# Kernel tuning notes

Hardware: AMD Instinct MI355X
Metric: run time of the kernel (lower is better)

The kernel has to match this reference:

```python
import jax, jax.numpy as jnp
import numpy as np

EMB = 512
QKV = 512
H = 8      # num_heads
PH = 8     # num_pheads
HD = QKV // H
PHD = QKV // PH


def _make_params(key):
    names = ['Wi', 'Wip', 'Wic', 'Wq', 'Wpq', 'Wk', 'Wpk', 'Wv', 'Wpv', 'Wo', 'Wop']
    ks = jax.random.split(key, len(names))
    p = {}
    for n, k in zip(names, ks):
        din = EMB if n in ('Wi', 'Wip', 'Wic') else QKV
        dout = EMB if n in ('Wo', 'Wop') else QKV
        p[n] = jax.random.normal(k, (din, dout), jnp.float32) * 0.02
        p['b' + n[1:]] = jnp.zeros((dout,), jnp.float32)
    return p


def setup_inputs() -> dict:
    key = jax.random.key(0)
    kq, kp, kc, kw = jax.random.split(key, 4)
    B, S, P = 16, 4096, 64
    inp = {
        'query': jax.random.normal(kq, (B, S, EMB), jnp.float32),
        'pquery': jax.random.normal(kp, (B, P, EMB), jnp.float32),
        'context': jax.random.normal(kc, (B, S, EMB), jnp.float32),
    }
    inp.update(_make_params(kw))
    return inp


def reference(query, pquery, context,
              Wi, bi, Wip, bip, Wic, bic,
              Wq, bq, Wpq, bpq, Wk, bk, Wpk, bpk,
              Wv, bv, Wpv, bpv, Wo, bo, Wop, bop):
    # Dropout layers act as identity (eval mode / deterministic reference).
    B, S, _ = query.shape
    P = pquery.shape[1]

    q_in = query @ Wi + bi        # (B,S,QKV)
    pq_in = pquery @ Wip + bip    # (B,P,QKV)
    c_in = context @ Wic + bic    # (B,S,QKV)

    # --- pack stage: pquery attends over context -> p_context ---
    pq = ((pq_in @ Wpq + bpq) * (PHD ** -0.5)).reshape(B, P, PH, PHD)
    pk = (c_in @ Wpk + bpk).reshape(B, S, PH, PHD)
    pv = (c_in @ Wpv + bpv).reshape(B, S, PH, PHD)
    # dropout before softmax in original; identity here
    pattn = jax.nn.softmax(jnp.einsum('bphd,bshd->bhps', pq, pk), axis=-1)
    pc = jnp.einsum('bhps,bshd->bphd', pattn, pv).reshape(B, P, QKV)

    # --- unpack stage: query attends over p_context ---
    q = ((q_in @ Wq + bq) * (HD ** -0.5)).reshape(B, S, H, HD)
    k = (pc @ Wk + bk).reshape(B, P, H, HD)
    v = (pc @ Wv + bv).reshape(B, P, H, HD)
    aw = jax.nn.softmax(jnp.einsum('bshd,bphd->bhsp', q, k), axis=-1)  # (B,H,S,P)
    attn = jnp.einsum('bhsp,bphd->bshd', aw, v).reshape(B, S, QKV)
    attn = attn @ Wo + bo           # (B,S,EMB)
    pc_out = pc @ Wop + bop         # (B,P,EMB)

    # torch returns attn_weights as (S, B*H, P) when batch_first
    aw_t = jnp.transpose(aw.reshape(B * H, S, P), (1, 0, 2))
    return attn, pc_out, aw_t
```

## Files before the change

kernel.cpp:

```cpp
#include <hip/hip_runtime.h>


typedef __bf16 bf16x8 __attribute__((ext_vector_type(8)));
typedef float f32x4 __attribute__((ext_vector_type(4)));
typedef unsigned short u16x8 __attribute__((ext_vector_type(8)));
typedef unsigned short u16x4 __attribute__((ext_vector_type(4)));

#define MFMA16(a, b, c) __builtin_amdgcn_mfma_f32_16x16x32_bf16((a), (b), (c), 0, 0, 0)

__device__ __forceinline__ unsigned short f2bf_bits(float f) {
  unsigned int u = __float_as_uint(f);
  u += 0x7fffu + ((u >> 16) & 1u);
  return (unsigned short)(u >> 16);
}

__device__ __forceinline__ void gload16(const unsigned short* g, unsigned short* l) {
  __builtin_amdgcn_global_load_lds(
      (const __attribute__((address_space(1))) void*)g,
      (__attribute__((address_space(3))) void*)l, 16, 0, 0);
}

struct Ptr8 { const float* p[8]; };

__global__ __launch_bounds__(256) void transpose_w8(Ptr8 srcs,
                                                    unsigned short* __restrict__ WT) {
  const float* __restrict__ W = srcs.p[blockIdx.z];
  unsigned short* __restrict__ O = WT + (size_t)blockIdx.z * 262144;
  __shared__ float tile[32][33];
  const int t = threadIdx.x;
  const int tr = blockIdx.x * 32, tc = blockIdx.y * 32;
  {
    const int r = t >> 3, c4 = (t & 7) * 4;
    const float4 v = *reinterpret_cast<const float4*>(&W[(size_t)(tr + r) * 512 + tc + c4]);
    tile[r][c4 + 0] = v.x; tile[r][c4 + 1] = v.y; tile[r][c4 + 2] = v.z; tile[r][c4 + 3] = v.w;
  }
  __syncthreads();
  {
    const int n = t >> 3, k4 = (t & 7) * 4;
    u16x4 o;
#pragma unroll
    for (int j = 0; j < 4; j++) o[j] = f2bf_bits(tile[k4 + j][n]);
    *reinterpret_cast<u16x4*>(&O[(size_t)(tc + n) * 512 + tr + k4]) = o;
  }
}

__global__ __launch_bounds__(256) void bias_all(
    const float* bi, const float* bip, const float* bic,
    const float* Wq, const float* Wpq, const float* Wpk, const float* Wpv,
    const float* bq, const float* bpq, const float* bpk, const float* bpv,
    float* __restrict__ out) {
  const int y = blockIdx.y;
  const float* bin  = (y == 0) ? bi : (y == 1) ? bip : bic;
  const float* W    = (y == 0) ? Wq : (y == 1) ? Wpq : (y == 2) ? Wpk : Wpv;
  const float* bout = (y == 0) ? bq : (y == 1) ? bpq : (y == 2) ? bpk : bpv;
  const float scale = (y < 2) ? 0.125f : 1.0f;
  const int n = blockIdx.x * 256 + threadIdx.x;
  float s = 0.f;
  for (int k = 0; k < 512; k++) s += bin[k] * W[(size_t)k * 512 + n];
  out[y * 512 + n] = (s + bout[n]) * scale;
}

__global__ __launch_bounds__(256) void gemm_wcomb(
    const float* __restrict__ Wi, const float* __restrict__ Wip,
    const float* __restrict__ Wic, const unsigned short* __restrict__ WTbase,
    unsigned short* __restrict__ outbase) {
  const int z = blockIdx.z;
  const float* __restrict__ A = (z == 0) ? Wi : (z == 1) ? Wip : Wic;
  const unsigned short* __restrict__ BT = WTbase + (size_t)z * 262144;
  unsigned short* __restrict__ out = outbase + (size_t)z * 262144;
  const float scale = (z < 2) ? 0.125f : 1.0f;

  __shared__ __align__(16) unsigned short As[128 * 72];
  __shared__ __align__(16) unsigned short Bs[128 * 72];
  const int t = threadIdx.x;
  const int w = t >> 6, l = t & 63, li = l & 15, lg = l >> 4;
  const int wm = w >> 1, wn = w & 1;
  const int m0 = blockIdx.x * 128, n0 = blockIdx.y * 128;

  f32x4 acc[4][4] = {};

  for (int kt = 0; kt < 512; kt += 64) {
#pragma unroll
    for (int i = 0; i < 8; i++) {
      const int row = i * 16 + (t >> 4), k = (t & 15) * 4;
      const float4 v = *reinterpret_cast<const float4*>(&A[(size_t)(m0 + row) * 512 + kt + k]);
      u16x4 o;
      o[0] = f2bf_bits(v.x); o[1] = f2bf_bits(v.y);
      o[2] = f2bf_bits(v.z); o[3] = f2bf_bits(v.w);
      *reinterpret_cast<u16x4*>(&As[row * 72 + k]) = o;
    }
#pragma unroll
    for (int i = 0; i < 4; i++) {
      const int row = i * 32 + (t >> 3), k = (t & 7) * 8;
      const u16x8 v = *reinterpret_cast<const u16x8*>(&BT[(size_t)(n0 + row) * 512 + kt + k]);
      *reinterpret_cast<u16x8*>(&Bs[row * 72 + k]) = v;
    }
    __syncthreads();
#pragma unroll
    for (int kk = 0; kk < 2; kk++) {
      bf16x8 a[4], b[4];
#pragma unroll
      for (int mf = 0; mf < 4; mf++)
        a[mf] = *reinterpret_cast<const bf16x8*>(&As[(wm * 64 + mf * 16 + li) * 72 + kk * 32 + lg * 8]);
#pragma unroll
      for (int nf = 0; nf < 4; nf++)
        b[nf] = *reinterpret_cast<const bf16x8*>(&Bs[(wn * 64 + nf * 16 + li) * 72 + kk * 32 + lg * 8]);
#pragma unroll
      for (int mf = 0; mf < 4; mf++)
#pragma unroll
        for (int nf = 0; nf < 4; nf++)
          acc[mf][nf] = MFMA16(a[mf], b[nf], acc[mf][nf]);
    }
    __syncthreads();
  }
  const int lg4 = lg * 4;
#pragma unroll
  for (int nf = 0; nf < 4; nf++) {
    const int col = n0 + wn * 64 + nf * 16 + li;
#pragma unroll
    for (int mf = 0; mf < 4; mf++) {
      const int row = m0 + wm * 64 + mf * 16 + lg4;
#pragma unroll
      for (int r = 0; r < 4; r++)
        out[(size_t)col * 512 + row + r] = f2bf_bits(acc[mf][nf][r] * scale);
    }
  }
}

__global__ __launch_bounds__(256) void conv_bf16(const float* __restrict__ q,
                                                 const float* __restrict__ c,
                                                 unsigned short* __restrict__ qo,
                                                 unsigned short* __restrict__ co) {
  const float* __restrict__ src = blockIdx.y ? c : q;
  unsigned short* __restrict__ dst = blockIdx.y ? co : qo;
#pragma unroll
  for (int i = 0; i < 8; i++) {
    const size_t idx = (((size_t)i * 2048 + blockIdx.x) * 256 + threadIdx.x) * 8;
    const float4 v0 = *reinterpret_cast<const float4*>(&src[idx]);
    const float4 v1 = *reinterpret_cast<const float4*>(&src[idx + 4]);
    u16x8 o;
    o[0] = f2bf_bits(v0.x); o[1] = f2bf_bits(v0.y); o[2] = f2bf_bits(v0.z); o[3] = f2bf_bits(v0.w);
    o[4] = f2bf_bits(v1.x); o[5] = f2bf_bits(v1.y); o[6] = f2bf_bits(v1.z); o[7] = f2bf_bits(v1.w);
    *reinterpret_cast<u16x8*>(&dst[idx]) = o;
  }
}

template <int MODE>
__global__ __launch_bounds__(256) void gemm_bf16(
    const unsigned short* __restrict__ A, const unsigned short* __restrict__ BT,
    const float* __restrict__ bias0, const float* __restrict__ bias1,
    const float* __restrict__ bias2, void* out0, void* out1, void* out2,
    int K, int Ntiles, int ldc) {
  __shared__ __align__(16) unsigned short As[128 * 64];
  __shared__ __align__(16) unsigned short Bs[128 * 64];
  const int t = threadIdx.x;
  const int w = t >> 6, l = t & 63, li = l & 15, lg = l >> 4;
  const int wm = w >> 1, wn = w & 1;

  const int q8 = gridDim.x >> 3;
  const int wg = (blockIdx.x & 7) * q8 + (blockIdx.x >> 3);
  const int m0 = (wg / Ntiles) * 128, n0 = (wg % Ntiles) * 128;

  f32x4 acc[4][4] = {};

  const int sr = t >> 3, sslot = t & 7;

  for (int kt = 0; kt < K; kt += 64) {
#pragma unroll
    for (int i = 0; i < 4; i++) {
      const int row = i * 32 + sr;
      const int gs = (sslot ^ (row & 7)) * 8;
      gload16(&A[(size_t)(m0 + row) * K + kt + gs], &As[(i * 256 + t) * 8]);
      gload16(&BT[(size_t)(n0 + row) * K + kt + gs], &Bs[(i * 256 + t) * 8]);
    }
    __syncthreads();
#pragma unroll
    for (int kk = 0; kk < 2; kk++) {
      bf16x8 a[4], b[4];
#pragma unroll
      for (int mf = 0; mf < 4; mf++) {
        const int r = wm * 64 + mf * 16 + li;
        a[mf] = *reinterpret_cast<const bf16x8*>(&As[r * 64 + (((kk * 4 + lg) ^ (r & 7)) * 8)]);
      }
#pragma unroll
      for (int nf = 0; nf < 4; nf++) {
        const int r = wn * 64 + nf * 16 + li;
        b[nf] = *reinterpret_cast<const bf16x8*>(&Bs[r * 64 + (((kk * 4 + lg) ^ (r & 7)) * 8)]);
      }
#pragma unroll
      for (int mf = 0; mf < 4; mf++)
#pragma unroll
        for (int nf = 0; nf < 4; nf++)
          acc[mf][nf] = MFMA16(a[mf], b[nf], acc[mf][nf]);
    }
    __syncthreads();
  }

  const int lg4 = lg * 4;
#pragma unroll
  for (int nf = 0; nf < 4; nf++) {
    const int col = n0 + wn * 64 + nf * 16 + li;
    if constexpr (MODE == 0) {
      unsigned short* o = (unsigned short*)out0;
      const float bv = bias0[col];
#pragma unroll
      for (int mf = 0; mf < 4; mf++) {
        const int row = m0 + wm * 64 + mf * 16 + lg4;
#pragma unroll
        for (int r = 0; r < 4; r++)
          o[(size_t)(row + r) * ldc + col] = f2bf_bits(acc[mf][nf][r] + bv);
      }
    } else if constexpr (MODE == 1) {
      float* o = (float*)out0;
      const float bv = bias0[col];
#pragma unroll
      for (int mf = 0; mf < 4; mf++) {
        const int row = m0 + wm * 64 + mf * 16 + lg4;
#pragma unroll
        for (int r = 0; r < 4; r++)
          o[(size_t)(row + r) * ldc + col] = acc[mf][nf][r] + bv;
      }
    } else {
      if (col < 512) {
        unsigned short* o = (unsigned short*)out0;
        const float bv = bias0[col];
#pragma unroll
        for (int mf = 0; mf < 4; mf++) {
          const int row = m0 + wm * 64 + mf * 16 + lg4;
#pragma unroll
          for (int r = 0; r < 4; r++)
            o[(size_t)(row + r) * 512 + col] = f2bf_bits(acc[mf][nf][r] + bv);
        }
      } else if (col < 1024) {
        unsigned short* o = (unsigned short*)out1;
        const float bv = bias1[col - 512];
#pragma unroll
        for (int mf = 0; mf < 4; mf++) {
          const int row = m0 + wm * 64 + mf * 16 + lg4;
#pragma unroll
          for (int r = 0; r < 4; r++)
            o[(size_t)(row + r) * 512 + col - 512] = f2bf_bits(acc[mf][nf][r] + bv);
        }
      } else {
        float* o = (float*)out2;
        const float bv = bias2[col - 1024];
#pragma unroll
        for (int mf = 0; mf < 4; mf++) {
          const int row = m0 + wm * 64 + mf * 16 + lg4;
#pragma unroll
          for (int r = 0; r < 4; r++)
            o[(size_t)(row + r) * 512 + col - 1024] = acc[mf][nf][r] + bv;
        }
      }
    }
  }
}

__global__ __launch_bounds__(256) void gemm_f32a(
    const float* __restrict__ A, const unsigned short* __restrict__ BT,
    const float* __restrict__ bias0, unsigned short* __restrict__ out,
    int K, int ldc) {
  __shared__ __align__(16) unsigned short As[128 * 72];
  __shared__ __align__(16) unsigned short Bs[128 * 72];
  const int t = threadIdx.x;
  const int w = t >> 6, l = t & 63, li = l & 15, lg = l >> 4;
  const int wm = w >> 1, wn = w & 1;
  const int m0 = blockIdx.x * 128, n0 = blockIdx.y * 128;

  f32x4 acc[4][4] = {};

  for (int kt = 0; kt < K; kt += 64) {
#pragma unroll
    for (int i = 0; i < 8; i++) {
      const int row = i * 16 + (t >> 4), k = (t & 15) * 4;
      const float4 v = *reinterpret_cast<const float4*>(&A[(size_t)(m0 + row) * K + kt + k]);
      u16x4 o;
      o[0] = f2bf_bits(v.x); o[1] = f2bf_bits(v.y);
      o[2] = f2bf_bits(v.z); o[3] = f2bf_bits(v.w);
      *reinterpret_cast<u16x4*>(&As[row * 72 + k]) = o;
    }
#pragma unroll
    for (int i = 0; i < 4; i++) {
      const int row = i * 32 + (t >> 3), k = (t & 7) * 8;
      const u16x8 v = *reinterpret_cast<const u16x8*>(&BT[(size_t)(n0 + row) * K + kt + k]);
      *reinterpret_cast<u16x8*>(&Bs[row * 72 + k]) = v;
    }
    __syncthreads();
#pragma unroll
    for (int kk = 0; kk < 2; kk++) {
      bf16x8 a[4], b[4];
#pragma unroll
      for (int mf = 0; mf < 4; mf++)
        a[mf] = *reinterpret_cast<const bf16x8*>(&As[(wm * 64 + mf * 16 + li) * 72 + kk * 32 + lg * 8]);
#pragma unroll
      for (int nf = 0; nf < 4; nf++)
        b[nf] = *reinterpret_cast<const bf16x8*>(&Bs[(wn * 64 + nf * 16 + li) * 72 + kk * 32 + lg * 8]);
#pragma unroll
      for (int mf = 0; mf < 4; mf++)
#pragma unroll
        for (int nf = 0; nf < 4; nf++)
          acc[mf][nf] = MFMA16(a[mf], b[nf], acc[mf][nf]);
    }
    __syncthreads();
  }
  const int lg4 = lg * 4;
#pragma unroll
  for (int nf = 0; nf < 4; nf++) {
    const int col = n0 + wn * 64 + nf * 16 + li;
    const float bv = bias0[col];
#pragma unroll
    for (int mf = 0; mf < 4; mf++) {
      const int row = m0 + wm * 64 + mf * 16 + lg4;
#pragma unroll
      for (int r = 0; r < 4; r++)
        out[(size_t)(row + r) * ldc + col] = f2bf_bits(acc[mf][nf][r] + bv);
    }
  }
}

__global__ __launch_bounds__(256) void pack_attn(
    const unsigned short* __restrict__ pq_buf,
    const unsigned short* __restrict__ pkv_buf, float* __restrict__ partial) {
  __shared__ __align__(16) unsigned short pkL[64 * 72];
  __shared__ __align__(16) unsigned short pvT[64 * 72];
  __shared__ __align__(16) unsigned short prL[4 * 16 * 72];
  const int t = threadIdx.x, w = t >> 6, l = t & 63, li = l & 15, lg = l >> 4;
  const int bh = blockIdx.x, b = bh >> 3, h = bh & 7;
  const int sb = blockIdx.y * 1024;

  bf16x8 aq[2];
  {
    const size_t base = ((size_t)(b * 64 + w * 16 + li)) * 512 + h * 64;
    aq[0] = *reinterpret_cast<const bf16x8*>(&pq_buf[base + lg * 8]);
    aq[1] = *reinterpret_cast<const bf16x8*>(&pq_buf[base + 32 + lg * 8]);
  }

  f32x4 acc[4] = {};
  float lsum[4] = {};

  for (int st = 0; st < 16; st++) {
    const int s0 = sb + st * 64;
#pragma unroll
    for (int i = 0; i < 2; i++) {
      const int row = i * 32 + (t >> 3), c = (t & 7) * 8;
      const u16x8 v = *reinterpret_cast<const u16x8*>(
          &pkv_buf[((size_t)(b * 4096 + s0 + row)) * 1024 + h * 64 + c]);
      *reinterpret_cast<u16x8*>(&pkL[row * 72 + c]) = v;
    }
    {
      const int rp = t >> 3, c = (t & 7) * 8;
      const size_t base = ((size_t)(b * 4096 + s0 + 2 * rp)) * 1024 + 512 + h * 64 + c;
      const u16x8 u0 = *reinterpret_cast<const u16x8*>(&pkv_buf[base]);
      const u16x8 u1 = *reinterpret_cast<const u16x8*>(&pkv_buf[base + 1024]);
#pragma unroll
      for (int j = 0; j < 8; j++) {
        const int val = ((int)u0[j] & 0xffff) | ((int)u1[j] << 16);
        *reinterpret_cast<int*>(&pvT[(c + j) * 72 + 2 * rp]) = val;
      }
    }
    __syncthreads();
    f32x4 sc[4] = {};
#pragma unroll
    for (int nf = 0; nf < 4; nf++) {
#pragma unroll
      for (int kk = 0; kk < 2; kk++) {
        const bf16x8 bk = *reinterpret_cast<const bf16x8*>(
            &pkL[(nf * 16 + li) * 72 + kk * 32 + lg * 8]);
        sc[nf] = MFMA16(aq[kk], bk, sc[nf]);
      }
    }
#pragma unroll
    for (int nf = 0; nf < 4; nf++) {
#pragma unroll
      for (int r = 0; r < 4; r++) {
        const float e = __expf(sc[nf][r]);
        lsum[r] += e;
        prL[(w * 16 + lg * 4 + r) * 72 + nf * 16 + li] = f2bf_bits(e);
      }
    }
#pragma unroll
    for (int kk = 0; kk < 2; kk++) {
      const bf16x8 ap = *reinterpret_cast<const bf16x8*>(
          &prL[(w * 16 + li) * 72 + kk * 32 + lg * 8]);
#pragma unroll
      for (int nf = 0; nf < 4; nf++) {
        const bf16x8 bv = *reinterpret_cast<const bf16x8*>(
            &pvT[(nf * 16 + li) * 72 + kk * 32 + lg * 8]);
        acc[nf] = MFMA16(ap, bv, acc[nf]);
      }
    }
    __syncthreads();
  }

#pragma unroll
  for (int m = 1; m < 16; m <<= 1)
#pragma unroll
    for (int r = 0; r < 4; r++) lsum[r] += __shfl_xor(lsum[r], m);

  const size_t pbase = ((size_t)(bh * 4 + blockIdx.y)) * 4160;
#pragma unroll
  for (int nf = 0; nf < 4; nf++)
#pragma unroll
    for (int r = 0; r < 4; r++)
      partial[pbase + (size_t)(w * 16 + lg * 4 + r) * 64 + nf * 16 + li] = acc[nf][r];
  if (li == 0)
#pragma unroll
    for (int r = 0; r < 4; r++) partial[pbase + 4096 + w * 16 + lg * 4 + r] = lsum[r];
}

__global__ __launch_bounds__(256) void pack_combine(const float* __restrict__ partial,
                                                    unsigned short* __restrict__ pc_buf) {
  const int bh = blockIdx.x, b = bh >> 3, h = bh & 7;
  const int t = threadIdx.x;
#pragma unroll
  for (int e = 0; e < 16; e++) {
    const int idx = e * 256 + t;
    const int p = idx >> 6, d = idx & 63;
    float s = 0.f, den = 0.f;
#pragma unroll
    for (int c = 0; c < 4; c++) {
      const float* pb = &partial[((size_t)(bh * 4 + c)) * 4160];
      s += pb[idx];
      den += pb[4096 + p];
    }
    pc_buf[((size_t)(b * 64 + p)) * 512 + h * 64 + d] = f2bf_bits(s / den);
  }
}

__global__ __launch_bounds__(256) void unpack_attn(
    const unsigned short* q_in, const unsigned short* __restrict__ k_buf,
    const unsigned short* __restrict__ v_buf, float* __restrict__ aw_out,
    unsigned short* attnh_out) {
  __shared__ __align__(16) unsigned short kL[64 * 72];
  __shared__ __align__(16) unsigned short vT[64 * 72];
  __shared__ __align__(16) unsigned short prL[4 * 64 * 72];
  const int t = threadIdx.x, w = t >> 6, l = t & 63, li = l & 15, lg = l >> 4;
  const int bh = blockIdx.y, b = bh >> 3, h = bh & 7;
  const int sbase = blockIdx.x * 256 + w * 64;

#pragma unroll
  for (int i = 0; i < 2; i++) {
    const int p = i * 32 + (t >> 3), c = (t & 7) * 8;
    const u16x8 v = *reinterpret_cast<const u16x8*>(
        &k_buf[((size_t)(b * 64 + p)) * 512 + h * 64 + c]);
    *reinterpret_cast<u16x8*>(&kL[p * 72 + c]) = v;
  }
  {
    const int rp = t >> 3, c = (t & 7) * 8;
    const size_t base = ((size_t)(b * 64 + 2 * rp)) * 512 + h * 64 + c;
    const u16x8 u0 = *reinterpret_cast<const u16x8*>(&v_buf[base]);
    const u16x8 u1 = *reinterpret_cast<const u16x8*>(&v_buf[base + 512]);
#pragma unroll
    for (int j = 0; j < 8; j++) {
      const int val = ((int)u0[j] & 0xffff) | ((int)u1[j] << 16);
      *reinterpret_cast<int*>(&vT[(c + j) * 72 + 2 * rp]) = val;
    }
  }
  bf16x8 aq[4][2];
#pragma unroll
  for (int mf = 0; mf < 4; mf++) {
    const size_t base = ((size_t)(b * 4096 + sbase + mf * 16 + li)) * 512 + h * 64;
    aq[mf][0] = *reinterpret_cast<const bf16x8*>(&q_in[base + lg * 8]);
    aq[mf][1] = *reinterpret_cast<const bf16x8*>(&q_in[base + 32 + lg * 8]);
  }
  __syncthreads();

  f32x4 sc[4][4] = {};
#pragma unroll
  for (int kk = 0; kk < 2; kk++)
#pragma unroll
    for (int nf = 0; nf < 4; nf++) {
      const bf16x8 bk = *reinterpret_cast<const bf16x8*>(
          &kL[(nf * 16 + li) * 72 + kk * 32 + lg * 8]);
#pragma unroll
      for (int mf = 0; mf < 4; mf++) sc[mf][nf] = MFMA16(aq[mf][kk], bk, sc[mf][nf]);
    }

#pragma unroll
  for (int mf = 0; mf < 4; mf++) {
#pragma unroll
    for (int r = 0; r < 4; r++) {
      float e[4];
      float rs = 0.f;
#pragma unroll
      for (int nf = 0; nf < 4; nf++) {
        e[nf] = __expf(sc[mf][nf][r]);
        rs += e[nf];
      }
#pragma unroll
      for (int m = 1; m < 16; m <<= 1) rs += __shfl_xor(rs, m);
      const float inv = 1.0f / rs;
      const int srow = sbase + mf * 16 + lg * 4 + r;
#pragma unroll
      for (int nf = 0; nf < 4; nf++) {
        const float pr = e[nf] * inv;
        aw_out[(size_t)srow * 8192 + bh * 64 + nf * 16 + li] = pr;
        prL[(w * 64 + mf * 16 + lg * 4 + r) * 72 + nf * 16 + li] = f2bf_bits(pr);
      }
    }
  }

  f32x4 acc[4][4] = {};
#pragma unroll
  for (int kk = 0; kk < 2; kk++)
#pragma unroll
    for (int mf = 0; mf < 4; mf++) {
      const bf16x8 ap = *reinterpret_cast<const bf16x8*>(
          &prL[(w * 64 + mf * 16 + li) * 72 + kk * 32 + lg * 8]);
#pragma unroll
      for (int nf = 0; nf < 4; nf++) {
        const bf16x8 bv = *reinterpret_cast<const bf16x8*>(
            &vT[(nf * 16 + li) * 72 + kk * 32 + lg * 8]);
        acc[mf][nf] = MFMA16(ap, bv, acc[mf][nf]);
      }
    }
#pragma unroll
  for (int mf = 0; mf < 4; mf++)
#pragma unroll
    for (int nf = 0; nf < 4; nf++)
#pragma unroll
      for (int r = 0; r < 4; r++)
        attnh_out[((size_t)(b * 4096 + sbase + mf * 16 + lg * 4 + r)) * 512 + h * 64 +
                  nf * 16 + li] = f2bf_bits(acc[mf][nf][r]);
}

extern "C" void kernel_launch(void* const* d_in, const int* in_sizes, int n_in,
                              void* d_out, int out_size, void* d_ws, size_t ws_size,
                              hipStream_t stream) {
  (void)in_sizes; (void)n_in; (void)out_size; (void)ws_size;

  const float* query   = (const float*)d_in[0];
  const float* pquery  = (const float*)d_in[1];
  const float* context = (const float*)d_in[2];
  const float* Wi  = (const float*)d_in[3];  const float* bi  = (const float*)d_in[4];
  const float* Wip = (const float*)d_in[5];  const float* bip = (const float*)d_in[6];
  const float* Wic = (const float*)d_in[7];  const float* bic = (const float*)d_in[8];
  const float* Wq  = (const float*)d_in[9];  const float* bq  = (const float*)d_in[10];
  const float* Wpq = (const float*)d_in[11]; const float* bpq = (const float*)d_in[12];
  const float* Wk  = (const float*)d_in[13]; const float* bk  = (const float*)d_in[14];
  const float* Wpk = (const float*)d_in[15]; const float* bpk = (const float*)d_in[16];
  const float* Wv  = (const float*)d_in[17]; const float* bv  = (const float*)d_in[18];
  const float* Wpv = (const float*)d_in[19]; const float* bpv = (const float*)d_in[20];
  const float* Wo  = (const float*)d_in[21]; const float* bo  = (const float*)d_in[22];
  const float* Wop = (const float*)d_in[23]; const float* bop = (const float*)d_in[24];

  char* ws = (char*)d_ws;
  unsigned short* WT     = (unsigned short*)(ws);
  unsigned short* WqeT   = (unsigned short*)(ws + 4u * 1024 * 1024);
  unsigned short* WpqeT  = WqeT + 512 * 512;
  unsigned short* WpkveT = WpqeT + 512 * 512;
  float* bqe   = (float*)(WpkveT + (size_t)1024 * 512);
  float* bpqe  = bqe + 512;
  float* bpkve = bpqe + 512;
  unsigned short* q_buf   = (unsigned short*)(ws + 8u * 1024 * 1024);
  unsigned short* pkv_buf = q_buf + (size_t)65536 * 512;
  unsigned short* pq_buf  = pkv_buf + (size_t)65536 * 1024;
  unsigned short* pc_buf  = pq_buf + (size_t)1024 * 512;
  unsigned short* k_buf   = pc_buf + (size_t)1024 * 512;
  unsigned short* v_buf   = k_buf + (size_t)1024 * 512;
  float* partial = (float*)(v_buf + (size_t)1024 * 512);

  float* out_attn = (float*)d_out;
  float* out_pc   = out_attn + (size_t)16 * 4096 * 512;
  float* out_aw   = out_pc + (size_t)16 * 64 * 512;

  unsigned short* c_bf = (unsigned short*)out_attn;
  unsigned short* q_bf = (unsigned short*)out_aw;

  const dim3 blk(256);

  Ptr8 tsrc; tsrc.p[0]=Wq; tsrc.p[1]=Wpq; tsrc.p[2]=Wpk; tsrc.p[3]=Wpv;
  tsrc.p[4]=Wk; tsrc.p[5]=Wv; tsrc.p[6]=Wop; tsrc.p[7]=Wo;
  transpose_w8<<<dim3(16, 16, 8), blk, 0, stream>>>(tsrc, WT);
  bias_all<<<dim3(2, 4), blk, 0, stream>>>(bi, bip, bic, Wq, Wpq, Wpk, Wpv,
                                           bq, bpq, bpk, bpv, bqe);
  gemm_wcomb<<<dim3(4, 4, 4), blk, 0, stream>>>(Wi, Wip, Wic, WT, WqeT);

  conv_bf16<<<dim3(2048, 2), blk, 0, stream>>>(query, context, q_bf, c_bf);

  gemm_bf16<0><<<dim3(2048), blk, 0, stream>>>(
      q_bf, WqeT, bqe, nullptr, nullptr, q_buf, nullptr, nullptr, 512, 4, 512);
  gemm_bf16<0><<<dim3(4096), blk, 0, stream>>>(
      c_bf, WpkveT, bpkve, nullptr, nullptr, pkv_buf, nullptr, nullptr, 512, 8, 1024);
  gemm_f32a<<<dim3(8, 4), blk, 0, stream>>>(pquery, WpqeT, bpqe, pq_buf, 512, 512);

  pack_attn<<<dim3(128, 4), blk, 0, stream>>>(pq_buf, pkv_buf, partial);
  pack_combine<<<128, blk, 0, stream>>>(partial, pc_buf);

  gemm_bf16<2><<<dim3(96), blk, 0, stream>>>(
      pc_buf, WT + (size_t)4 * 262144, bk, bv, bop, k_buf, v_buf, out_pc, 512, 12, 512);

  unpack_attn<<<dim3(16, 128), blk, 0, stream>>>(q_buf, k_buf, v_buf, out_aw, q_buf);

  gemm_bf16<1><<<dim3(2048), blk, 0, stream>>>(
      q_buf, WT + (size_t)7 * 262144, bo, nullptr, nullptr, out_attn, nullptr, nullptr,
      512, 4, 512);
}
```

Before: 560.8 us.

## Fuse fp32-to-bf16 input conversion into register-fed GEMM with wide N tiles

Removes the separate conv_bf16 pass over query and context. A new GEMM kernel reads fp32 A rows directly into registers, converts them to bf16 on the fly and prefetches the next K slice, while B tiles are double-buffered in LDS. Each 512-thread block covers a 128x512 output tile, so A is read once per row block. The pack attention split across S is doubled from 4 to 8 chunks for more parallelism, at the cost of a larger combine step. Larger LDS use (128KB) and more registers may limit occupancy.

```diff
diff --git a/kernel.cpp b/kernel.cpp
--- a/kernel.cpp
+++ b/kernel.cpp
@@ -127,42 +127,144 @@
   }
 }
 
-__global__ __launch_bounds__(256) void conv_bf16(const float* __restrict__ q,
-                                                 const float* __restrict__ c,
-                                                 unsigned short* __restrict__ qo,
-                                                 unsigned short* __restrict__ co) {
-  const float* __restrict__ src = blockIdx.y ? c : q;
-  unsigned short* __restrict__ dst = blockIdx.y ? co : qo;
+template <typename AT, int MODE, int NT>
+__global__ __launch_bounds__(512) void gemm_fa(
+    const AT* __restrict__ A, const unsigned short* __restrict__ BT,
+    const float* __restrict__ bias0, void* out0, int ldc) {
+  __shared__ __align__(16) unsigned short Bs[2][512 * 64];
+  const int t = threadIdx.x;
+  const int w = t >> 6, l = t & 63, li = l & 15, lg = l >> 4;
+  const int wm = w >> 2, wn = w & 3;
+  const int bid = blockIdx.x;
+  const int m0 = (bid / NT) * 128, n0 = (bid % NT) * 512;
+  const int K = 512;
+
+  f32x4 acc[4][8] = {};
+
+  const int st_row_base = (t >> 3);
+  const int st_slot = t & 7;
+
 #pragma unroll
   for (int i = 0; i < 8; i++) {
-    const size_t idx = (((size_t)i * 2048 + blockIdx.x) * 256 + threadIdx.x) * 8;
-    const float4 v0 = *reinterpret_cast<const float4*>(&src[idx]);
-    const float4 v1 = *reinterpret_cast<const float4*>(&src[idx + 4]);
-    u16x8 o;
-    o[0] = f2bf_bits(v0.x); o[1] = f2bf_bits(v0.y); o[2] = f2bf_bits(v0.z); o[3] = f2bf_bits(v0.w);
-    o[4] = f2bf_bits(v1.x); o[5] = f2bf_bits(v1.y); o[6] = f2bf_bits(v1.z); o[7] = f2bf_bits(v1.w);
-    *reinterpret_cast<u16x8*>(&dst[idx]) = o;
-  }
-}
-
-template <int MODE>
-__global__ __launch_bounds__(256) void gemm_bf16(
+    const int row = i * 64 + st_row_base;
+    const int gs = (st_slot ^ (row & 7)) * 8;
+    gload16(&BT[(size_t)(n0 + row) * K + gs], &Bs[0][(i * 512 + t) * 8]);
+  }
+
+  float4 a0f[4][2][2];
+  u16x8  a0b[4][2];
+#pragma unroll
+  for (int mf = 0; mf < 4; mf++) {
+    const size_t rbase = (size_t)(m0 + wm * 64 + mf * 16 + li) * K;
+#pragma unroll
+    for (int kk = 0; kk < 2; kk++) {
+      if constexpr (sizeof(AT) == 4) {
+        const float* src = (const float*)&A[rbase + kk * 32 + lg * 8];
+        a0f[mf][kk][0] = *reinterpret_cast<const float4*>(src);
+        a0f[mf][kk][1] = *reinterpret_cast<const float4*>(src + 4);
+      } else {
+        a0b[mf][kk] = *reinterpret_cast<const u16x8*>(&A[rbase + kk * 32 + lg * 8]);
+      }
+    }
+  }
+  __syncthreads();
+
+  for (int kt = 0; kt < K; kt += 64) {
+    const int cur = (kt >> 6) & 1;
+    const bool more = (kt + 64) < K;
+    if (more) {
+#pragma unroll
+      for (int i = 0; i < 8; i++) {
+        const int row = i * 64 + st_row_base;
+        const int gs = (st_slot ^ (row & 7)) * 8;
+        gload16(&BT[(size_t)(n0 + row) * K + kt + 64 + gs], &Bs[cur ^ 1][(i * 512 + t) * 8]);
+      }
+    }
+    bf16x8 af[4][2];
+#pragma unroll
+    for (int mf = 0; mf < 4; mf++)
+#pragma unroll
+      for (int kk = 0; kk < 2; kk++) {
+        if constexpr (sizeof(AT) == 4) {
+          bf16x8 v;
+#pragma unroll
+          for (int j = 0; j < 4; j++) {
+            v[j]     = (__bf16)a0f[mf][kk][0][j];
+            v[j + 4] = (__bf16)a0f[mf][kk][1][j];
+          }
+          af[mf][kk] = v;
+        } else {
+          af[mf][kk] = *reinterpret_cast<const bf16x8*>(&a0b[mf][kk]);
+        }
+      }
+    if (more) {
+#pragma unroll
+      for (int mf = 0; mf < 4; mf++) {
+        const size_t rbase = (size_t)(m0 + wm * 64 + mf * 16 + li) * K + kt + 64;
+#pragma unroll
+        for (int kk = 0; kk < 2; kk++) {
+          if constexpr (sizeof(AT) == 4) {
+            const float* src = (const float*)&A[rbase + kk * 32 + lg * 8];
+            a0f[mf][kk][0] = *reinterpret_cast<const float4*>(src);
+            a0f[mf][kk][1] = *reinterpret_cast<const float4*>(src + 4);
+          } else {
+            a0b[mf][kk] = *reinterpret_cast<const u16x8*>(&A[rbase + kk * 32 + lg * 8]);
+          }
+        }
+      }
+    }
+#pragma unroll
+    for (int kk = 0; kk < 2; kk++) {
+#pragma unroll
+      for (int nf = 0; nf < 8; nf++) {
+        const int row = wn * 128 + nf * 16 + li;
+        const bf16x8 b = *reinterpret_cast<const bf16x8*>(
+            &Bs[cur][row * 64 + (((kk * 4 + lg) ^ (row & 7)) * 8)]);
+#pragma unroll
+        for (int mf = 0; mf < 4; mf++)
+          acc[mf][nf] = MFMA16(af[mf][kk], b, acc[mf][nf]);
+      }
+    }
+    __syncthreads();
+  }
+
+  const int lg4 = lg * 4;
+#pragma unroll
+  for (int nf = 0; nf < 8; nf++) {
+    const int col = n0 + wn * 128 + nf * 16 + li;
+    const float bv = bias0[col];
+#pragma unroll
+    for (int mf = 0; mf < 4; mf++) {
+      const int row = m0 + wm * 64 + mf * 16 + lg4;
+      if constexpr (MODE == 0) {
+        unsigned short* o = (unsigned short*)out0;
+#pragma unroll
+        for (int r = 0; r < 4; r++)
+          o[(size_t)(row + r) * ldc + col] = f2bf_bits(acc[mf][nf][r] + bv);
+      } else {
+        float* o = (float*)out0;
+#pragma unroll
+        for (int r = 0; r < 4; r++)
+          o[(size_t)(row + r) * ldc + col] = acc[mf][nf][r] + bv;
+      }
+    }
+  }
+}
+
+__global__ __launch_bounds__(256) void gemm_kvpc(
     const unsigned short* __restrict__ A, const unsigned short* __restrict__ BT,
     const float* __restrict__ bias0, const float* __restrict__ bias1,
-    const float* __restrict__ bias2, void* out0, void* out1, void* out2,
-    int K, int Ntiles, int ldc) {
+    const float* __restrict__ bias2, unsigned short* out0, unsigned short* out1,
+    float* out2, int Ntiles) {
   __shared__ __align__(16) unsigned short As[128 * 64];
   __shared__ __align__(16) unsigned short Bs[128 * 64];
   const int t = threadIdx.x;
   const int w = t >> 6, l = t & 63, li = l & 15, lg = l >> 4;
   const int wm = w >> 1, wn = w & 1;
-
-  const int q8 = gridDim.x >> 3;
-  const int wg = (blockIdx.x & 7) * q8 + (blockIdx.x >> 3);
-  const int m0 = (wg / Ntiles) * 128, n0 = (wg % Ntiles) * 128;
+  const int K = 512;
+  const int m0 = (blockIdx.x / Ntiles) * 128, n0 = (blockIdx.x % Ntiles) * 128;
 
   f32x4 acc[4][4] = {};
-
   const int sr = t >> 3, sslot = t & 7;
 
   for (int kt = 0; kt < K; kt += 64) {
@@ -200,57 +302,32 @@
 #pragma unroll
   for (int nf = 0; nf < 4; nf++) {
     const int col = n0 + wn * 64 + nf * 16 + li;
-    if constexpr (MODE == 0) {
-      unsigned short* o = (unsigned short*)out0;
+    if (col < 512) {
       const float bv = bias0[col];
 #pragma unroll
       for (int mf = 0; mf < 4; mf++) {
         const int row = m0 + wm * 64 + mf * 16 + lg4;
 #pragma unroll
         for (int r = 0; r < 4; r++)
-          o[(size_t)(row + r) * ldc + col] = f2bf_bits(acc[mf][nf][r] + bv);
-      }
-    } else if constexpr (MODE == 1) {
-      float* o = (float*)out0;
-      const float bv = bias0[col];
+          out0[(size_t)(row + r) * 512 + col] = f2bf_bits(acc[mf][nf][r] + bv);
+      }
+    } else if (col < 1024) {
+      const float bv = bias1[col - 512];
 #pragma unroll
       for (int mf = 0; mf < 4; mf++) {
         const int row = m0 + wm * 64 + mf * 16 + lg4;
 #pragma unroll
         for (int r = 0; r < 4; r++)
-          o[(size_t)(row + r) * ldc + col] = acc[mf][nf][r] + bv;
+          out1[(size_t)(row + r) * 512 + col - 512] = f2bf_bits(acc[mf][nf][r] + bv);
       }
     } else {
-      if (col < 512) {
-        unsigned short* o = (unsigned short*)out0;
-        const float bv = bias0[col];
-#pragma unroll
-        for (int mf = 0; mf < 4; mf++) {
-          const int row = m0 + wm * 64 + mf * 16 + lg4;
-#pragma unroll
-          for (int r = 0; r < 4; r++)
-            o[(size_t)(row + r) * 512 + col] = f2bf_bits(acc[mf][nf][r] + bv);
-        }
-      } else if (col < 1024) {
-        unsigned short* o = (unsigned short*)out1;
-        const float bv = bias1[col - 512];
-#pragma unroll
-        for (int mf = 0; mf < 4; mf++) {
-          const int row = m0 + wm * 64 + mf * 16 + lg4;
-#pragma unroll
-          for (int r = 0; r < 4; r++)
-            o[(size_t)(row + r) * 512 + col - 512] = f2bf_bits(acc[mf][nf][r] + bv);
-        }
-      } else {
-        float* o = (float*)out2;
-        const float bv = bias2[col - 1024];
-#pragma unroll
-        for (int mf = 0; mf < 4; mf++) {
-          const int row = m0 + wm * 64 + mf * 16 + lg4;
-#pragma unroll
-          for (int r = 0; r < 4; r++)
-            o[(size_t)(row + r) * 512 + col - 1024] = acc[mf][nf][r] + bv;
-        }
+      const float bv = bias2[col - 1024];
+#pragma unroll
+      for (int mf = 0; mf < 4; mf++) {
+        const int row = m0 + wm * 64 + mf * 16 + lg4;
+#pragma unroll
+        for (int r = 0; r < 4; r++)
+          out2[(size_t)(row + r) * 512 + col - 1024] = acc[mf][nf][r] + bv;
       }
     }
   }
@@ -326,7 +403,7 @@
   __shared__ __align__(16) unsigned short prL[4 * 16 * 72];
   const int t = threadIdx.x, w = t >> 6, l = t & 63, li = l & 15, lg = l >> 4;
   const int bh = blockIdx.x, b = bh >> 3, h = bh & 7;
-  const int sb = blockIdx.y * 1024;
+  const int sb = blockIdx.y * 512;
 
   bf16x8 aq[2];
   {
@@ -338,7 +415,7 @@
   f32x4 acc[4] = {};
   float lsum[4] = {};
 
-  for (int st = 0; st < 16; st++) {
+  for (int st = 0; st < 8; st++) {
     const int s0 = sb + st * 64;
 #pragma unroll
     for (int i = 0; i < 2; i++) {
@@ -397,7 +474,7 @@
 #pragma unroll
     for (int r = 0; r < 4; r++) lsum[r] += __shfl_xor(lsum[r], m);
 
-  const size_t pbase = ((size_t)(bh * 4 + blockIdx.y)) * 4160;
+  const size_t pbase = ((size_t)(bh * 8 + blockIdx.y)) * 4160;
 #pragma unroll
   for (int nf = 0; nf < 4; nf++)
 #pragma unroll
@@ -418,8 +495,8 @@
     const int p = idx >> 6, d = idx & 63;
     float s = 0.f, den = 0.f;
 #pragma unroll
-    for (int c = 0; c < 4; c++) {
-      const float* pb = &partial[((size_t)(bh * 4 + c)) * 4160];
+    for (int c = 0; c < 8; c++) {
+      const float* pb = &partial[((size_t)(bh * 8 + c)) * 4160];
       s += pb[idx];
       den += pb[4096 + p];
     }
@@ -564,10 +641,8 @@
   float* out_pc   = out_attn + (size_t)16 * 4096 * 512;
   float* out_aw   = out_pc + (size_t)16 * 64 * 512;
 
-  unsigned short* c_bf = (unsigned short*)out_attn;
-  unsigned short* q_bf = (unsigned short*)out_aw;
-
   const dim3 blk(256);
+  const dim3 blk512(512);
 
   Ptr8 tsrc; tsrc.p[0]=Wq; tsrc.p[1]=Wpq; tsrc.p[2]=Wpk; tsrc.p[3]=Wpv;
   tsrc.p[4]=Wk; tsrc.p[5]=Wv; tsrc.p[6]=Wop; tsrc.p[7]=Wo;
@@ -576,23 +651,20 @@
                                            bq, bpq, bpk, bpv, bqe);
   gemm_wcomb<<<dim3(4, 4, 4), blk, 0, stream>>>(Wi, Wip, Wic, WT, WqeT);
 
-  conv_bf16<<<dim3(2048, 2), blk, 0, stream>>>(query, context, q_bf, c_bf);
-
-  gemm_bf16<0><<<dim3(2048), blk, 0, stream>>>(
-      q_bf, WqeT, bqe, nullptr, nullptr, q_buf, nullptr, nullptr, 512, 4, 512);
-  gemm_bf16<0><<<dim3(4096), blk, 0, stream>>>(
-      c_bf, WpkveT, bpkve, nullptr, nullptr, pkv_buf, nullptr, nullptr, 512, 8, 1024);
+  gemm_fa<float, 0, 1><<<dim3(512), blk512, 0, stream>>>(
+      query, WqeT, bqe, q_buf, 512);
+  gemm_fa<float, 0, 2><<<dim3(1024), blk512, 0, stream>>>(
+      context, WpkveT, bpkve, pkv_buf, 1024);
   gemm_f32a<<<dim3(8, 4), blk, 0, stream>>>(pquery, WpqeT, bpqe, pq_buf, 512, 512);
 
-  pack_attn<<<dim3(128, 4), blk, 0, stream>>>(pq_buf, pkv_buf, partial);
+  pack_attn<<<dim3(128, 8), blk, 0, stream>>>(pq_buf, pkv_buf, partial);
   pack_combine<<<128, blk, 0, stream>>>(partial, pc_buf);
 
-  gemm_bf16<2><<<dim3(96), blk, 0, stream>>>(
-      pc_buf, WT + (size_t)4 * 262144, bk, bv, bop, k_buf, v_buf, out_pc, 512, 12, 512);
+  gemm_kvpc<<<dim3(96), blk, 0, stream>>>(
+      pc_buf, WT + (size_t)4 * 262144, bk, bv, bop, k_buf, v_buf, out_pc, 12);
 
   unpack_attn<<<dim3(16, 128), blk, 0, stream>>>(q_buf, k_buf, v_buf, out_aw, q_buf);
 
-  gemm_bf16<1><<<dim3(2048), blk, 0, stream>>>(
-      q_buf, WT + (size_t)7 * 262144, bo, nullptr, nullptr, out_attn, nullptr, nullptr,
-      512, 4, 512);
-}
+  gemm_fa<unsigned short, 1, 1><<<dim3(512), blk512, 0, stream>>>(
+      q_buf, WT + (size_t)7 * 262144, bo, out_attn, 512);
+}
```

After: 805.3 us. +43.6%, slower.

## Fuse fp32-to-bf16 conversion into input GEMMs and widen pack split

Applied to the files above, without the earlier changes.

Drops the separate conv_bf16 pass over query and context. The input GEMMs now load fp32 tiles straight into LDS with a swizzle and convert them to bf16 while building MFMA fragments, which removes a full read-write round trip of two 128MB tensors. The weight transpose and bias kernels are merged into one launch, and the pack attention sequence split goes from 4 to 8 chunks for more parallelism. In exchange, the fp32 A tile doubles LDS traffic and footprint per block, which may lower occupancy.

```diff
diff --git a/kernel.cpp b/kernel.cpp
--- a/kernel.cpp
+++ b/kernel.cpp
@@ -14,7 +14,7 @@
   return (unsigned short)(u >> 16);
 }
 
-__device__ __forceinline__ void gload16(const unsigned short* g, unsigned short* l) {
+__device__ __forceinline__ void gload16(const void* g, void* l) {
   __builtin_amdgcn_global_load_lds(
       (const __attribute__((address_space(1))) void*)g,
       (__attribute__((address_space(3))) void*)l, 16, 0, 0);
@@ -22,42 +22,44 @@
 
 struct Ptr8 { const float* p[8]; };
 
-__global__ __launch_bounds__(256) void transpose_w8(Ptr8 srcs,
-                                                    unsigned short* __restrict__ WT) {
-  const float* __restrict__ W = srcs.p[blockIdx.z];
-  unsigned short* __restrict__ O = WT + (size_t)blockIdx.z * 262144;
-  __shared__ float tile[32][33];
-  const int t = threadIdx.x;
-  const int tr = blockIdx.x * 32, tc = blockIdx.y * 32;
-  {
-    const int r = t >> 3, c4 = (t & 7) * 4;
-    const float4 v = *reinterpret_cast<const float4*>(&W[(size_t)(tr + r) * 512 + tc + c4]);
-    tile[r][c4 + 0] = v.x; tile[r][c4 + 1] = v.y; tile[r][c4 + 2] = v.z; tile[r][c4 + 3] = v.w;
-  }
-  __syncthreads();
-  {
-    const int n = t >> 3, k4 = (t & 7) * 4;
-    u16x4 o;
-#pragma unroll
-    for (int j = 0; j < 4; j++) o[j] = f2bf_bits(tile[k4 + j][n]);
-    *reinterpret_cast<u16x4*>(&O[(size_t)(tc + n) * 512 + tr + k4]) = o;
-  }
-}
-
-__global__ __launch_bounds__(256) void bias_all(
+__global__ __launch_bounds__(256) void prep_kernel(
+    Ptr8 srcs, unsigned short* __restrict__ WT,
     const float* bi, const float* bip, const float* bic,
     const float* Wq, const float* Wpq, const float* Wpk, const float* Wpv,
     const float* bq, const float* bpq, const float* bpk, const float* bpv,
-    float* __restrict__ out) {
-  const int y = blockIdx.y;
-  const float* bin  = (y == 0) ? bi : (y == 1) ? bip : bic;
-  const float* W    = (y == 0) ? Wq : (y == 1) ? Wpq : (y == 2) ? Wpk : Wpv;
-  const float* bout = (y == 0) ? bq : (y == 1) ? bpq : (y == 2) ? bpk : bpv;
-  const float scale = (y < 2) ? 0.125f : 1.0f;
-  const int n = blockIdx.x * 256 + threadIdx.x;
-  float s = 0.f;
-  for (int k = 0; k < 512; k++) s += bin[k] * W[(size_t)k * 512 + n];
-  out[y * 512 + n] = (s + bout[n]) * scale;
+    float* __restrict__ bias_out) {
+  const int t = threadIdx.x;
+  if (blockIdx.z < 8) {
+    const float* __restrict__ W = srcs.p[blockIdx.z];
+    unsigned short* __restrict__ O = WT + (size_t)blockIdx.z * 262144;
+    __shared__ float tile[32][33];
+    const int tr = blockIdx.x * 32, tc = blockIdx.y * 32;
+    {
+      const int r = t >> 3, c4 = (t & 7) * 4;
+      const float4 v = *reinterpret_cast<const float4*>(&W[(size_t)(tr + r) * 512 + tc + c4]);
+      tile[r][c4 + 0] = v.x; tile[r][c4 + 1] = v.y; tile[r][c4 + 2] = v.z; tile[r][c4 + 3] = v.w;
+    }
+    __syncthreads();
+    {
+      const int n = t >> 3, k4 = (t & 7) * 4;
+      u16x4 o;
+#pragma unroll
+      for (int j = 0; j < 4; j++) o[j] = f2bf_bits(tile[k4 + j][n]);
+      *reinterpret_cast<u16x4*>(&O[(size_t)(tc + n) * 512 + tr + k4]) = o;
+    }
+  } else {
+    const int idx = blockIdx.y * 16 + blockIdx.x;
+    if (idx >= 8) return;
+    const int y = idx >> 1;
+    const float* bin  = (y == 0) ? bi : (y == 1) ? bip : bic;
+    const float* W    = (y == 0) ? Wq : (y == 1) ? Wpq : (y == 2) ? Wpk : Wpv;
+    const float* bout = (y == 0) ? bq : (y == 1) ? bpq : (y == 2) ? bpk : bpv;
+    const float scale = (y < 2) ? 0.125f : 1.0f;
+    const int n = (idx & 1) * 256 + t;
+    float s = 0.f;
+    for (int k = 0; k < 512; k++) s += bin[k] * W[(size_t)k * 512 + n];
+    bias_out[y * 512 + n] = (s + bout[n]) * scale;
+  }
 }
 
 __global__ __launch_bounds__(256) void gemm_wcomb(
@@ -127,21 +129,80 @@
   }
 }
 
-__global__ __launch_bounds__(256) void conv_bf16(const float* __restrict__ q,
-                                                 const float* __restrict__ c,
-                                                 unsigned short* __restrict__ qo,
-                                                 unsigned short* __restrict__ co) {
-  const float* __restrict__ src = blockIdx.y ? c : q;
-  unsigned short* __restrict__ dst = blockIdx.y ? co : qo;
-#pragma unroll
-  for (int i = 0; i < 8; i++) {
-    const size_t idx = (((size_t)i * 2048 + blockIdx.x) * 256 + threadIdx.x) * 8;
-    const float4 v0 = *reinterpret_cast<const float4*>(&src[idx]);
-    const float4 v1 = *reinterpret_cast<const float4*>(&src[idx + 4]);
-    u16x8 o;
-    o[0] = f2bf_bits(v0.x); o[1] = f2bf_bits(v0.y); o[2] = f2bf_bits(v0.z); o[3] = f2bf_bits(v0.w);
-    o[4] = f2bf_bits(v1.x); o[5] = f2bf_bits(v1.y); o[6] = f2bf_bits(v1.z); o[7] = f2bf_bits(v1.w);
-    *reinterpret_cast<u16x8*>(&dst[idx]) = o;
+__global__ __launch_bounds__(256) void gemm_f32lds(
+    const float* __restrict__ A, const unsigned short* __restrict__ BT,
+    const float* __restrict__ bias0, unsigned short* __restrict__ out0,
+    int Ntiles, int ldc) {
+  __shared__ __align__(16) float Asf[128 * 64];
+  __shared__ __align__(16) unsigned short Bs[128 * 64];
+  const int t = threadIdx.x;
+  const int w = t >> 6, l = t & 63, li = l & 15, lg = l >> 4;
+  const int wm = w >> 1, wn = w & 1;
+  const int K = 512;
+
+  const int q8 = gridDim.x >> 3;
+  const int wg = (blockIdx.x & 7) * q8 + (blockIdx.x >> 3);
+  const int m0 = (wg / Ntiles) * 128, n0 = (wg % Ntiles) * 128;
+
+  f32x4 acc[4][4] = {};
+
+  const int arow = t >> 4, aslot = t & 15;
+  const int brow = t >> 3, bslot = t & 7;
+
+  for (int kt = 0; kt < K; kt += 64) {
+#pragma unroll
+    for (int i = 0; i < 8; i++) {
+      const int row = i * 16 + arow;
+      const int gs = (aslot ^ (row & 15)) * 4;
+      gload16(&A[(size_t)(m0 + row) * K + kt + gs], &Asf[i * 1024 + t * 4]);
+    }
+#pragma unroll
+    for (int i = 0; i < 4; i++) {
+      const int row = i * 32 + brow;
+      const int gs = (bslot ^ (row & 7)) * 8;
+      gload16(&BT[(size_t)(n0 + row) * K + kt + gs], &Bs[(i * 256 + t) * 8]);
+    }
+    __syncthreads();
+#pragma unroll
+    for (int kk = 0; kk < 2; kk++) {
+      bf16x8 a[4], b[4];
+#pragma unroll
+      for (int mf = 0; mf < 4; mf++) {
+        const int r = wm * 64 + mf * 16 + li;
+        const int s0 = kk * 8 + lg * 2;
+        const f32x4 lo = *reinterpret_cast<const f32x4*>(&Asf[r * 64 + ((s0 ^ (r & 15)) * 4)]);
+        const f32x4 hi = *reinterpret_cast<const f32x4*>(&Asf[r * 64 + (((s0 + 1) ^ (r & 15)) * 4)]);
+        bf16x8 v;
+#pragma unroll
+        for (int j = 0; j < 4; j++) { v[j] = (__bf16)lo[j]; v[j + 4] = (__bf16)hi[j]; }
+        a[mf] = v;
+      }
+#pragma unroll
+      for (int nf = 0; nf < 4; nf++) {
+        const int r = wn * 64 + nf * 16 + li;
+        b[nf] = *reinterpret_cast<const bf16x8*>(&Bs[r * 64 + (((kk * 4 + lg) ^ (r & 7)) * 8)]);
+      }
+#pragma unroll
+      for (int mf = 0; mf < 4; mf++)
+#pragma unroll
+        for (int nf = 0; nf < 4; nf++)
+          acc[mf][nf] = MFMA16(a[mf], b[nf], acc[mf][nf]);
+    }
+    __syncthreads();
+  }
+
+  const int lg4 = lg * 4;
+#pragma unroll
+  for (int nf = 0; nf < 4; nf++) {
+    const int col = n0 + wn * 64 + nf * 16 + li;
+    const float bv = bias0[col];
+#pragma unroll
+    for (int mf = 0; mf < 4; mf++) {
+      const int row = m0 + wm * 64 + mf * 16 + lg4;
+#pragma unroll
+      for (int r = 0; r < 4; r++)
+        out0[(size_t)(row + r) * ldc + col] = f2bf_bits(acc[mf][nf][r] + bv);
+    }
   }
 }
 
@@ -150,19 +211,19 @@
     const unsigned short* __restrict__ A, const unsigned short* __restrict__ BT,
     const float* __restrict__ bias0, const float* __restrict__ bias1,
     const float* __restrict__ bias2, void* out0, void* out1, void* out2,
-    int K, int Ntiles, int ldc) {
+    int Ntiles, int ldc) {
   __shared__ __align__(16) unsigned short As[128 * 64];
   __shared__ __align__(16) unsigned short Bs[128 * 64];
   const int t = threadIdx.x;
   const int w = t >> 6, l = t & 63, li = l & 15, lg = l >> 4;
   const int wm = w >> 1, wn = w & 1;
+  const int K = 512;
 
   const int q8 = gridDim.x >> 3;
   const int wg = (blockIdx.x & 7) * q8 + (blockIdx.x >> 3);
   const int m0 = (wg / Ntiles) * 128, n0 = (wg % Ntiles) * 128;
 
   f32x4 acc[4][4] = {};
-
   const int sr = t >> 3, sslot = t & 7;
 
   for (int kt = 0; kt < K; kt += 64) {
@@ -200,17 +261,7 @@
 #pragma unroll
   for (int nf = 0; nf < 4; nf++) {
     const int col = n0 + wn * 64 + nf * 16 + li;
-    if constexpr (MODE == 0) {
-      unsigned short* o = (unsigned short*)out0;
-      const float bv = bias0[col];
-#pragma unroll
-      for (int mf = 0; mf < 4; mf++) {
-        const int row = m0 + wm * 64 + mf * 16 + lg4;
-#pragma unroll
-        for (int r = 0; r < 4; r++)
-          o[(size_t)(row + r) * ldc + col] = f2bf_bits(acc[mf][nf][r] + bv);
-      }
-    } else if constexpr (MODE == 1) {
+    if constexpr (MODE == 1) {
       float* o = (float*)out0;
       const float bv = bias0[col];
 #pragma unroll
@@ -326,7 +377,7 @@
   __shared__ __align__(16) unsigned short prL[4 * 16 * 72];
   const int t = threadIdx.x, w = t >> 6, l = t & 63, li = l & 15, lg = l >> 4;
   const int bh = blockIdx.x, b = bh >> 3, h = bh & 7;
-  const int sb = blockIdx.y * 1024;
+  const int sb = blockIdx.y * 512;
 
   bf16x8 aq[2];
   {
@@ -338,7 +389,7 @@
   f32x4 acc[4] = {};
   float lsum[4] = {};
 
-  for (int st = 0; st < 16; st++) {
+  for (int st = 0; st < 8; st++) {
     const int s0 = sb + st * 64;
 #pragma unroll
     for (int i = 0; i < 2; i++) {
@@ -397,7 +448,7 @@
 #pragma unroll
     for (int r = 0; r < 4; r++) lsum[r] += __shfl_xor(lsum[r], m);
 
-  const size_t pbase = ((size_t)(bh * 4 + blockIdx.y)) * 4160;
+  const size_t pbase = ((size_t)(bh * 8 + blockIdx.y)) * 4160;
 #pragma unroll
   for (int nf = 0; nf < 4; nf++)
 #pragma unroll
@@ -418,8 +469,8 @@
     const int p = idx >> 6, d = idx & 63;
     float s = 0.f, den = 0.f;
 #pragma unroll
-    for (int c = 0; c < 4; c++) {
-      const float* pb = &partial[((size_t)(bh * 4 + c)) * 4160];
+    for (int c = 0; c < 8; c++) {
+      const float* pb = &partial[((size_t)(bh * 8 + c)) * 4160];
       s += pb[idx];
       den += pb[4096 + p];
     }
@@ -564,35 +615,27 @@
   float* out_pc   = out_attn + (size_t)16 * 4096 * 512;
   float* out_aw   = out_pc + (size_t)16 * 64 * 512;
 
-  unsigned short* c_bf = (unsigned short*)out_attn;
-  unsigned short* q_bf = (unsigned short*)out_aw;
-
   const dim3 blk(256);
 
   Ptr8 tsrc; tsrc.p[0]=Wq; tsrc.p[1]=Wpq; tsrc.p[2]=Wpk; tsrc.p[3]=Wpv;
   tsrc.p[4]=Wk; tsrc.p[5]=Wv; tsrc.p[6]=Wop; tsrc.p[7]=Wo;
-  transpose_w8<<<dim3(16, 16, 8), blk, 0, stream>>>(tsrc, WT);
-  bias_all<<<dim3(2, 4), blk, 0, stream>>>(bi, bip, bic, Wq, Wpq, Wpk, Wpv,
-                                           bq, bpq, bpk, bpv, bqe);
+  prep_kernel<<<dim3(16, 16, 9), blk, 0, stream>>>(
+      tsrc, WT, bi, bip, bic, Wq, Wpq, Wpk, Wpv, bq, bpq, bpk, bpv, bqe);
   gemm_wcomb<<<dim3(4, 4, 4), blk, 0, stream>>>(Wi, Wip, Wic, WT, WqeT);
 
-  conv_bf16<<<dim3(2048, 2), blk, 0, stream>>>(query, context, q_bf, c_bf);
-
-  gemm_bf16<0><<<dim3(2048), blk, 0, stream>>>(
-      q_bf, WqeT, bqe, nullptr, nullptr, q_buf, nullptr, nullptr, 512, 4, 512);
-  gemm_bf16<0><<<dim3(4096), blk, 0, stream>>>(
-      c_bf, WpkveT, bpkve, nullptr, nullptr, pkv_buf, nullptr, nullptr, 512, 8, 1024);
+  gemm_f32lds<<<dim3(2048), blk, 0, stream>>>(query, WqeT, bqe, q_buf, 4, 512);
+  gemm_f32lds<<<dim3(4096), blk, 0, stream>>>(context, WpkveT, bpkve, pkv_buf, 8, 1024);
   gemm_f32a<<<dim3(8, 4), blk, 0, stream>>>(pquery, WpqeT, bpqe, pq_buf, 512, 512);
 
-  pack_attn<<<dim3(128, 4), blk, 0, stream>>>(pq_buf, pkv_buf, partial);
+  pack_attn<<<dim3(128, 8), blk, 0, stream>>>(pq_buf, pkv_buf, partial);
   pack_combine<<<128, blk, 0, stream>>>(partial, pc_buf);
 
   gemm_bf16<2><<<dim3(96), blk, 0, stream>>>(
-      pc_buf, WT + (size_t)4 * 262144, bk, bv, bop, k_buf, v_buf, out_pc, 512, 12, 512);
+      pc_buf, WT + (size_t)4 * 262144, bk, bv, bop, k_buf, v_buf, out_pc, 12, 512);
 
   unpack_attn<<<dim3(16, 128), blk, 0, stream>>>(q_buf, k_buf, v_buf, out_aw, q_buf);
 
   gemm_bf16<1><<<dim3(2048), blk, 0, stream>>>(
       q_buf, WT + (size_t)7 * 262144, bo, nullptr, nullptr, out_attn, nullptr, nullptr,
-      512, 4, 512);
-}
+      4, 512);
+}
```

After: 525.7 us. -6.3%, faster.
